# Kernel optimization log

Hardware: AMD Instinct MI355X
Metric: run time of the kernel (lower is better)

The kernel has to match this reference:

```python
import jax, jax.numpy as jnp
import numpy as np

T, K = 2048, 6          # tokens, activated experts per token
DIM = 2048              # model dim
INTER = 1408            # moe intermediate dim
E = 16                  # routed experts (group_size, shared not fused)


def setup_inputs() -> dict:
    key = jax.random.key(0)
    k1, k2, k3, k4, k5, k6 = jax.random.split(key, 6)
    x = jax.random.normal(k1, (T, DIM), dtype=jnp.float32)
    weights = jax.random.uniform(k2, (T, K), dtype=jnp.float32)
    indices = jax.random.randint(k3, (T, K), 0, E, dtype=jnp.int64)
    s = 1.0 / np.sqrt(DIM)
    Wg = jax.random.normal(k4, (E, INTER, DIM), dtype=jnp.float32) * s
    Wu = jax.random.normal(k5, (E, INTER, DIM), dtype=jnp.float32) * s
    Wd = jax.random.normal(k6, (E, DIM, INTER), dtype=jnp.float32) * (1.0 / np.sqrt(INTER))
    return {"x": x, "weights": weights, "indices": indices,
            "Wg": Wg, "Wu": Wu, "Wd": Wd}


def reference(x, weights, indices, Wg, Wu, Wd):
    # per-token combine weight for each expert: [T, E]
    # gate_w[t, e] = sum_k weights[t, k] * (indices[t, k] == e)
    one_hot = jax.nn.one_hot(indices, E, dtype=x.dtype)        # [T, K, E]
    gate_w = jnp.einsum('tk,tke->te', weights, one_hot)        # [T, E]

    # SwiGLU expert FFN, dense over experts, combine folded pre-down-proj
    g = jnp.einsum('td,eid->tei', x, Wg)                       # [T, E, INTER]
    u = jnp.einsum('td,eid->tei', x, Wu)                       # [T, E, INTER]
    act = jax.nn.silu(g) * u                                   # [T, E, INTER]
    # y[t] = sum_e gate_w[t,e] * (act[t,e] @ Wd[e].T)
    y = jnp.einsum('tei,edi->td', act * gate_w[:, :, None], Wd)  # [T, DIM]
    return y
```

## Files before the change

kernel.cpp:

```cpp
#include <hip/hip_runtime.h>
#include <hip/hip_bf16.h>
#include <cstdint>

#define TT     2048
#define KSEL   6
#define DMODEL 2048
#define DINTER 1408
#define NE     16
#define PMAX   (TT * KSEL)

typedef short bf16x8 __attribute__((ext_vector_type(8)));
typedef float f32x4 __attribute__((ext_vector_type(4)));
typedef unsigned short u16;
typedef u16 u16x8 __attribute__((ext_vector_type(8)));

__device__ __forceinline__ u16 f2bf(float f) {
  union { float f; unsigned u; } v; v.f = f;
  return (u16)((v.u + 0x7FFFu + ((v.u >> 16) & 1u)) >> 16);
}
__device__ __forceinline__ float bf2f(u16 h) {
  union { unsigned u; float f; } v; v.u = (unsigned)h << 16; return v.f;
}

__device__ __forceinline__ void gl2lds16(const void* g, void* l) {
  __builtin_amdgcn_global_load_lds((const __attribute__((address_space(1))) void*)g,
                                   (__attribute__((address_space(3))) void*)l,
                                   16, 0, 0);
}

__global__ void k_gate(const float* __restrict__ w, const int* __restrict__ idx,
                       float* __restrict__ gate_w, int* __restrict__ counts) {
  int g = blockIdx.x * 256 + threadIdx.x;
  int t = g >> 4, e = g & 15;
  const int* ip = idx + t * KSEL;
  const float* wp = w + t * KSEL;
  float s = 0.f;
#pragma unroll
  for (int k = 0; k < KSEL; ++k) s += (ip[k] == e) ? wp[k] : 0.f;
  gate_w[g] = s;
  if (s != 0.f) atomicAdd(counts + e, 1);
}

__global__ void k_scan(const int* __restrict__ counts, int* __restrict__ offs) {
  if (threadIdx.x == 0 && blockIdx.x == 0) {
    int r = 0;
#pragma unroll
    for (int e = 0; e < NE; ++e) { offs[e] = r; r += counts[e]; }
    offs[NE] = r;
  }
}

__global__ void k_fill(const float* __restrict__ gate_w, const int* __restrict__ offs,
                       int* __restrict__ cursor, int* __restrict__ slot_tok,
                       float* __restrict__ slot_gate, int* __restrict__ tcnt,
                       int* __restrict__ tok_slots) {
  int g = blockIdx.x * 256 + threadIdx.x;
  int t = g >> 4, e = g & 15;
  float s = gate_w[g];
  if (s != 0.f) {
    int p = atomicAdd(cursor + e, 1);
    int sl = offs[e] + p;
    slot_tok[sl] = t;
    slot_gate[sl] = s;
    int q = atomicAdd(tcnt + t, 1);
    tok_slots[t * KSEL + q] = sl;
  }
}

#define XV8   (TT * DMODEL / 8)
#define WV8   (NE * DINTER * DMODEL / 8)
__global__ void k_castall(const float* __restrict__ x,  u16* __restrict__ xb,
                          const float* __restrict__ wg, u16* __restrict__ wgb,
                          const float* __restrict__ wu, u16* __restrict__ wub,
                          const float* __restrict__ wd, u16* __restrict__ wdb) {
  const int total = XV8 + 3 * WV8;
  int stride = gridDim.x * 256;
  for (int i = blockIdx.x * 256 + threadIdx.x; i < total; i += stride) {
    const float* src; u16* dst; int j;
    if (i < XV8)                { src = x;  dst = xb;  j = i; }
    else if (i < XV8 + WV8)     { src = wg; dst = wgb; j = i - XV8; }
    else if (i < XV8 + 2 * WV8) { src = wu; dst = wub; j = i - XV8 - WV8; }
    else                        { src = wd; dst = wdb; j = i - XV8 - 2 * WV8; }
    const float4* p = (const float4*)src + (size_t)j * 2;
    float4 v0 = p[0], v1 = p[1];
    u16x8 o;
    o[0] = f2bf(v0.x); o[1] = f2bf(v0.y); o[2] = f2bf(v0.z); o[3] = f2bf(v0.w);
    o[4] = f2bf(v1.x); o[5] = f2bf(v1.y); o[6] = f2bf(v1.z); o[7] = f2bf(v1.w);
    *(u16x8*)(dst + (size_t)j * 8) = o;
  }
}


__global__ __launch_bounds__(256, 2) void k_gemm1(
    const u16* __restrict__ xb, const u16* __restrict__ wgb, const u16* __restrict__ wub,
    const int* __restrict__ slot_tok, const float* __restrict__ slot_gate,
    const int* __restrict__ offs, const int* __restrict__ counts,
    u16* __restrict__ act) {
  int b = blockIdx.x;
  int w = (b & 7) * 352 + (b >> 3);
  int mt = w & 15, rest = w >> 4;
  int it = rest % 11, e = rest / 11;

  int mcount = counts[e];
  if (mt * 128 >= mcount) return;
  int mrem = mcount - mt * 128; if (mrem > 128) mrem = 128;
  int slotBase = offs[e] + mt * 128;
  int iBase = it * 128;

  __shared__ u16 sA[128 * 64];
  __shared__ u16 sG[128 * 64];
  __shared__ u16 sU[128 * 64];
  __shared__ int tokLds[128];
  __shared__ float gateLds[128];

  int tid = threadIdx.x;
  if (tid < 128) {
    int rl = tid < mrem ? tid : 0;
    tokLds[tid] = slot_tok[slotBase + rl];
    gateLds[tid] = (tid < mrem) ? slot_gate[slotBase + rl] : 0.f;
  }
  __syncthreads();

  int wv = tid >> 6, lane = tid & 63;
  const u16 *aSrc[4], *gSrc[4], *uSrc[4];
  u16 *aDst[4], *gDst[4], *uDst[4];
  const u16* gBase = wgb + ((size_t)e * DINTER + iBase) * DMODEL;
  const u16* uBase = wub + ((size_t)e * DINTER + iBase) * DMODEL;
  int r8 = lane >> 3;
  int colOff = ((lane & 7) ^ r8) * 8;
#pragma unroll
  for (int i2 = 0; i2 < 4; ++i2) {
    int chunk = wv * 4 + i2;
    int row = chunk * 8 + r8;
    aSrc[i2] = xb + (size_t)tokLds[row] * DMODEL + colOff;
    gSrc[i2] = gBase + (size_t)row * DMODEL + colOff;
    uSrc[i2] = uBase + (size_t)row * DMODEL + colOff;
    aDst[i2] = sA + chunk * 512;
    gDst[i2] = sG + chunk * 512;
    uDst[i2] = sU + chunk * 512;
  }

  f32x4 accg[4][4] = {};
  f32x4 accu[4][4] = {};
  int fr = lane & 15, fq = lane >> 4;
  int wr = (wv >> 1) * 64, wc = (wv & 1) * 64;

  for (int kb = 0; kb < DMODEL / 64; ++kb) {
    int kOff = kb * 64;
    __syncthreads();
#pragma unroll
    for (int i2 = 0; i2 < 4; ++i2) {
      gl2lds16(aSrc[i2] + kOff, aDst[i2]);
      gl2lds16(gSrc[i2] + kOff, gDst[i2]);
      gl2lds16(uSrc[i2] + kOff, uDst[i2]);
    }
    __syncthreads();
#pragma unroll
    for (int kf = 0; kf < 2; ++kf) {
      bf16x8 af[4], bg[4], bu[4];
#pragma unroll
      for (int mf = 0; mf < 4; ++mf) {
        int row = wr + mf * 16 + fr;
        int cu = ((kf * 4 + fq) ^ (row & 7)) * 8;
        af[mf] = *(const bf16x8*)&sA[row * 64 + cu];
      }
#pragma unroll
      for (int nf = 0; nf < 4; ++nf) {
        int row = wc + nf * 16 + fr;
        int cu = ((kf * 4 + fq) ^ (row & 7)) * 8;
        bg[nf] = *(const bf16x8*)&sG[row * 64 + cu];
        bu[nf] = *(const bf16x8*)&sU[row * 64 + cu];
      }
#pragma unroll
      for (int mf = 0; mf < 4; ++mf)
#pragma unroll
        for (int nf = 0; nf < 4; ++nf) {
          accg[mf][nf] = __builtin_amdgcn_mfma_f32_16x16x32_bf16(af[mf], bg[nf], accg[mf][nf], 0, 0, 0);
          accu[mf][nf] = __builtin_amdgcn_mfma_f32_16x16x32_bf16(af[mf], bu[nf], accu[mf][nf], 0, 0, 0);
        }
    }
  }
#pragma unroll
  for (int mf = 0; mf < 4; ++mf)
#pragma unroll
    for (int nf = 0; nf < 4; ++nf)
#pragma unroll
      for (int r = 0; r < 4; ++r) {
        int row = wr + mf * 16 + fq * 4 + r;
        if (row < mrem) {
          float g = accg[mf][nf][r], u = accu[mf][nf][r];
          float a = g / (1.f + __expf(-g)) * u * gateLds[row];
          act[(size_t)(slotBase + row) * DINTER + iBase + wc + nf * 16 + fr] = f2bf(a);
        }
      }
}

__global__ __launch_bounds__(256, 3) void k_gemm2(
    const u16* __restrict__ act, const u16* __restrict__ wdb,
    const int* __restrict__ slot_tok, const int* __restrict__ offs,
    const int* __restrict__ counts, float* __restrict__ y,
    u16* __restrict__ outb) {
  int b = blockIdx.x;
  int w = (b & 7) * 512 + (b >> 3);
  int mt = w & 15, rest = w >> 4;
  int dt = rest & 15, e = rest >> 4;

  int mcount = counts[e];
  if (mt * 128 >= mcount) return;
  int mrem = mcount - mt * 128; if (mrem > 128) mrem = 128;
  int slotBase = offs[e] + mt * 128;
  int dBase = dt * 128;

  __shared__ u16 sA[128 * 64];
  __shared__ u16 sB[128 * 64];
  __shared__ int tokLds[128];

  int tid = threadIdx.x;
  if (tid < 128) tokLds[tid] = slot_tok[slotBase + (tid < mrem ? tid : 0)];
  __syncthreads();

  int wv = tid >> 6, lane = tid & 63;
  const u16 *aSrc[4], *bSrc[4];
  u16 *aDst[4], *bDst[4];
  const u16* bBase = wdb + ((size_t)e * DMODEL + dBase) * DINTER;
  int r8 = lane >> 3;
  int colOff = ((lane & 7) ^ r8) * 8;
#pragma unroll
  for (int i2 = 0; i2 < 4; ++i2) {
    int chunk = wv * 4 + i2;
    int row = chunk * 8 + r8;
    aSrc[i2] = act + (size_t)(slotBase + row) * DINTER + colOff;
    bSrc[i2] = bBase + (size_t)row * DINTER + colOff;
    aDst[i2] = sA + chunk * 512;
    bDst[i2] = sB + chunk * 512;
  }

  f32x4 acc[4][4] = {};
  int fr = lane & 15, fq = lane >> 4;
  int wr = (wv >> 1) * 64, wc = (wv & 1) * 64;

  for (int kb = 0; kb < DINTER / 64; ++kb) {
    int kOff = kb * 64;
    __syncthreads();
#pragma unroll
    for (int i2 = 0; i2 < 4; ++i2) {
      gl2lds16(aSrc[i2] + kOff, aDst[i2]);
      gl2lds16(bSrc[i2] + kOff, bDst[i2]);
    }
    __syncthreads();
#pragma unroll
    for (int kf = 0; kf < 2; ++kf) {
      bf16x8 af[4], bb[4];
#pragma unroll
      for (int mf = 0; mf < 4; ++mf) {
        int row = wr + mf * 16 + fr;
        int cu = ((kf * 4 + fq) ^ (row & 7)) * 8;
        af[mf] = *(const bf16x8*)&sA[row * 64 + cu];
      }
#pragma unroll
      for (int nf = 0; nf < 4; ++nf) {
        int row = wc + nf * 16 + fr;
        int cu = ((kf * 4 + fq) ^ (row & 7)) * 8;
        bb[nf] = *(const bf16x8*)&sB[row * 64 + cu];
      }
#pragma unroll
      for (int mf = 0; mf < 4; ++mf)
#pragma unroll
        for (int nf = 0; nf < 4; ++nf)
          acc[mf][nf] = __builtin_amdgcn_mfma_f32_16x16x32_bf16(af[mf], bb[nf], acc[mf][nf], 0, 0, 0);
    }
  }
#pragma unroll
  for (int mf = 0; mf < 4; ++mf)
#pragma unroll
    for (int nf = 0; nf < 4; ++nf)
#pragma unroll
      for (int r = 0; r < 4; ++r) {
        int row = wr + mf * 16 + fq * 4 + r;
        if (row < mrem) {
          int col = dBase + wc + nf * 16 + fr;
          if (outb) {
            outb[(size_t)(slotBase + row) * DMODEL + col] = f2bf(acc[mf][nf][r]);
          } else {
            atomicAdd(y + (size_t)tokLds[row] * DMODEL + col, acc[mf][nf][r]);
          }
        }
      }
}

__global__ void k_combine(const u16* __restrict__ outb, const int* __restrict__ tok_slots,
                          const int* __restrict__ tcnt, float* __restrict__ y) {
  int idx = blockIdx.x * 256 + threadIdx.x;
  int t = idx >> 8;
  int d0 = (idx & 255) * 8;
  int n = tcnt[t];
  float s[8] = {};
  for (int j = 0; j < n; ++j) {
    int sl = tok_slots[t * KSEL + j];
    u16x8 v = *(const u16x8*)(outb + (size_t)sl * DMODEL + d0);
#pragma unroll
    for (int q = 0; q < 8; ++q) s[q] += bf2f(v[q]);
  }
  float4* yp = (float4*)(y + (size_t)t * DMODEL + d0);
  yp[0] = make_float4(s[0], s[1], s[2], s[3]);
  yp[1] = make_float4(s[4], s[5], s[6], s[7]);
}

extern "C" void kernel_launch(void* const* d_in, const int* in_sizes, int n_in,
                              void* d_out, int out_size, void* d_ws, size_t ws_size,
                              hipStream_t stream) {
  const float* x       = (const float*)d_in[0];
  const float* weights = (const float*)d_in[1];
  const int*   indices = (const int*)d_in[2];
  const float* Wg      = (const float*)d_in[3];
  const float* Wu      = (const float*)d_in[4];
  const float* Wd      = (const float*)d_in[5];
  float* y = (float*)d_out;

  const size_t WELEM = (size_t)NE * DINTER * DMODEL;

  char* ws = (char*)d_ws;
  size_t o = 0;
  float* gate_w = (float*)(ws + o); o += (size_t)TT * NE * 4;
  size_t ctrlOff = o;
  int* counts = (int*)(ws + o);
  int* offs   = (int*)(ws + o + 64);
  int* cursor = (int*)(ws + o + 192);
  int* tcnt   = (int*)(ws + o + 256);
  int* tok_slots = (int*)(ws + o + 256 + TT * 4);
  size_t ctrlZero = 256 + TT * 4;
  o += 256 + TT * 4 + (size_t)TT * KSEL * 4;
  int*   slot_tok  = (int*)(ws + o);   o += (size_t)PMAX * 4;
  float* slot_gate = (float*)(ws + o); o += (size_t)PMAX * 4;
  u16* xb  = (u16*)(ws + o); o += (size_t)TT * DMODEL * 2;
  u16* act = (u16*)(ws + o); o += (size_t)(PMAX + 128) * DINTER * 2;
  u16* wgb = (u16*)(ws + o); o += WELEM * 2;
  u16* wub = (u16*)(ws + o); o += WELEM * 2;
  u16* wdb = (u16*)(ws + o); o += WELEM * 2;
  u16* outb = (u16*)(ws + o);
  size_t oEnd = o + (size_t)PMAX * DMODEL * 2;
  bool useCombine = (ws_size >= oEnd);
  (void)in_sizes; (void)n_in;

  hipMemsetAsync(d_out, 0, (size_t)out_size * 4, stream);
  hipMemsetAsync(ws + ctrlOff, 0, ctrlZero, stream);

  k_gate<<<TT * NE / 256, 256, 0, stream>>>(weights, indices, gate_w, counts);
  k_scan<<<1, 64, 0, stream>>>(counts, offs);
  k_fill<<<TT * NE / 256, 256, 0, stream>>>(gate_w, offs, cursor, slot_tok, slot_gate,
                                            tcnt, tok_slots);
  k_castall<<<2048, 256, 0, stream>>>(x, xb, Wg, wgb, Wu, wub, Wd, wdb);
  k_gemm1<<<2816, 256, 0, stream>>>(xb, wgb, wub, slot_tok, slot_gate, offs, counts, act);
  k_gemm2<<<4096, 256, 0, stream>>>(act, wdb, slot_tok, offs, counts, y,
                                    useCombine ? outb : (u16*)nullptr);
  if (useCombine) {
    k_combine<<<TT * DMODEL / 8 / 256, 256, 0, stream>>>(outb, tok_slots, tcnt, y);
  }
}
```

Before: 581.2 us.

## Overlap Wd bf16 cast with gate/up GEMM by interleaving cast blocks

Moves the down-projection weight fp32->bf16 conversion out of the standalone cast kernel and into extra blocks of the first GEMM launch, interleaved one cast block per four GEMM blocks. The memory-bound cast is meant to run alongside the compute-bound MFMA blocks instead of serially before them, shrinking the cast kernel by a quarter. The risk is that the extra blocks compete for CU slots and bandwidth with the GEMM and change its block-to-tile mapping.

```diff
diff --git a/kernel.cpp b/kernel.cpp
--- a/kernel.cpp
+++ b/kernel.cpp
@@ -69,18 +69,16 @@
 
 #define XV8   (TT * DMODEL / 8)
 #define WV8   (NE * DINTER * DMODEL / 8)
-__global__ void k_castall(const float* __restrict__ x,  u16* __restrict__ xb,
-                          const float* __restrict__ wg, u16* __restrict__ wgb,
-                          const float* __restrict__ wu, u16* __restrict__ wub,
-                          const float* __restrict__ wd, u16* __restrict__ wdb) {
-  const int total = XV8 + 3 * WV8;
+__global__ void k_cast3(const float* __restrict__ x,  u16* __restrict__ xb,
+                        const float* __restrict__ wg, u16* __restrict__ wgb,
+                        const float* __restrict__ wu, u16* __restrict__ wub) {
+  const int total = XV8 + 2 * WV8;
   int stride = gridDim.x * 256;
   for (int i = blockIdx.x * 256 + threadIdx.x; i < total; i += stride) {
     const float* src; u16* dst; int j;
-    if (i < XV8)                { src = x;  dst = xb;  j = i; }
-    else if (i < XV8 + WV8)     { src = wg; dst = wgb; j = i - XV8; }
-    else if (i < XV8 + 2 * WV8) { src = wu; dst = wub; j = i - XV8 - WV8; }
-    else                        { src = wd; dst = wdb; j = i - XV8 - 2 * WV8; }
+    if (i < XV8)            { src = x;  dst = xb;  j = i; }
+    else if (i < XV8 + WV8) { src = wg; dst = wgb; j = i - XV8; }
+    else                    { src = wu; dst = wub; j = i - XV8 - WV8; }
     const float4* p = (const float4*)src + (size_t)j * 2;
     float4 v0 = p[0], v1 = p[1];
     u16x8 o;
@@ -93,11 +91,28 @@
 
 __global__ __launch_bounds__(256, 2) void k_gemm1(
     const u16* __restrict__ xb, const u16* __restrict__ wgb, const u16* __restrict__ wub,
+    const float* __restrict__ Wd, u16* __restrict__ wdb,
     const int* __restrict__ slot_tok, const float* __restrict__ slot_gate,
     const int* __restrict__ offs, const int* __restrict__ counts,
     u16* __restrict__ act) {
-  int b = blockIdx.x;
-  int w = (b & 7) * 352 + (b >> 3);
+  int bq = blockIdx.x >> 3, br = blockIdx.x & 7;
+  if (bq % 5 == 4) {
+    int c = (bq / 5) * 8 + br;
+    int base = c * 8192;
+#pragma unroll 4
+    for (int it = 0; it < 32; ++it) {
+      int j = base + it * 256 + threadIdx.x;
+      const float4* p = (const float4*)Wd + (size_t)j * 2;
+      float4 v0 = p[0], v1 = p[1];
+      u16x8 o;
+      o[0] = f2bf(v0.x); o[1] = f2bf(v0.y); o[2] = f2bf(v0.z); o[3] = f2bf(v0.w);
+      o[4] = f2bf(v1.x); o[5] = f2bf(v1.y); o[6] = f2bf(v1.z); o[7] = f2bf(v1.w);
+      *(u16x8*)(wdb + (size_t)j * 8) = o;
+    }
+    return;
+  }
+  int g = ((bq / 5) * 4 + (bq % 5)) * 8 + br;
+  int w = (g & 7) * 352 + (g >> 3);
   int mt = w & 15, rest = w >> 4;
   int it = rest % 11, e = rest / 11;
 
@@ -188,8 +203,8 @@
       for (int r = 0; r < 4; ++r) {
         int row = wr + mf * 16 + fq * 4 + r;
         if (row < mrem) {
-          float g = accg[mf][nf][r], u = accu[mf][nf][r];
-          float a = g / (1.f + __expf(-g)) * u * gateLds[row];
+          float gv = accg[mf][nf][r], uv = accu[mf][nf][r];
+          float a = gv / (1.f + __expf(-gv)) * uv * gateLds[row];
           act[(size_t)(slotBase + row) * DINTER + iBase + wc + nf * 16 + fr] = f2bf(a);
         }
       }
@@ -349,8 +364,9 @@
   k_scan<<<1, 64, 0, stream>>>(counts, offs);
   k_fill<<<TT * NE / 256, 256, 0, stream>>>(gate_w, offs, cursor, slot_tok, slot_gate,
                                             tcnt, tok_slots);
-  k_castall<<<2048, 256, 0, stream>>>(x, xb, Wg, wgb, Wu, wub, Wd, wdb);
-  k_gemm1<<<2816, 256, 0, stream>>>(xb, wgb, wub, slot_tok, slot_gate, offs, counts, act);
+  k_cast3<<<2048, 256, 0, stream>>>(x, xb, Wg, wgb, Wu, wub);
+  k_gemm1<<<3520, 256, 0, stream>>>(xb, wgb, wub, Wd, wdb, slot_tok, slot_gate,
+                                    offs, counts, act);
   k_gemm2<<<4096, 256, 0, stream>>>(act, wdb, slot_tok, offs, counts, y,
                                     useCombine ? outb : (u16*)nullptr);
   if (useCombine) {
```

Result: faster. 557.4 us (-4.1%).
